# Performance work log

Measured on AMD Instinct MI355X. Metric: run time of the kernel, lower is better.

The kernel has to match this reference:

```python
import jax, jax.numpy as jnp
import numpy as np
from jax import lax
from functools import partial


def _dilate(masks):
    # conv with an all-ones k x k kernel followed by (>0) == binary max-pool dilation
    H = masks.shape[-1]
    k = H // 50
    k = k if k % 2 == 1 else k + 1
    pad = k // 2
    d = lax.reduce_window(masks, -jnp.inf, lax.max, (1, 1, k, k), (1, 1, 1, 1),
                          [(0, 0), (0, 0), (pad, pad), (pad, pad)])
    return (d > 0).astype(masks.dtype)


def _boxes_from_masks(masks):
    # vectorized version of the torch double loop with per-mask torch.where
    N, M, H, W = masks.shape
    b = masks > 0
    any_y = b.any(axis=3)  # (N,M,H)
    any_x = b.any(axis=2)  # (N,M,W)
    ys = jnp.arange(H)
    xs = jnp.arange(W)
    ymin = jnp.min(jnp.where(any_y, ys, H), axis=-1)
    ymax = jnp.max(jnp.where(any_y, ys, -1), axis=-1)
    xmin = jnp.min(jnp.where(any_x, xs, W), axis=-1)
    xmax = jnp.max(jnp.where(any_x, xs, -1), axis=-1)
    x1 = jnp.maximum(0, xmin - 1)
    y1 = jnp.maximum(0, ymin - 1)
    x2 = jnp.minimum(W - 1, xmax + 1)
    y2 = jnp.minimum(H - 1, ymax + 1)
    box = jnp.stack([x1, y1, x2, y2], axis=-1).astype(jnp.float32)  # (N,M,4)
    nonempty = any_y.any(axis=-1)
    return jnp.where(nonempty[..., None], box, 0.0)


def _bilinear(feat, y, x):
    # torchvision roi_align bilinear sampling semantics (aligned=False)
    C, H, W = feat.shape
    valid = (y > -1.0) & (y < H) & (x > -1.0) & (x < W)
    y = jnp.clip(y, 0.0, H - 1.0)
    x = jnp.clip(x, 0.0, W - 1.0)
    y0 = jnp.floor(y).astype(jnp.int32)
    x0 = jnp.floor(x).astype(jnp.int32)
    y1 = jnp.minimum(y0 + 1, H - 1)
    x1 = jnp.minimum(x0 + 1, W - 1)
    ly = y - y0
    lx = x - x0
    hy = 1.0 - ly
    hx = 1.0 - lx
    v00 = feat[:, y0, x0]
    v01 = feat[:, y0, x1]
    v10 = feat[:, y1, x0]
    v11 = feat[:, y1, x1]
    val = hy * hx * v00 + hy * lx * v01 + ly * hx * v10 + ly * lx * v11
    return jnp.where(valid, val, 0.0)


def _roi_align_one(feat, box, R):
    # sampling_ratio=1: one sample at each bin center
    x1, y1, x2, y2 = box
    bw = jnp.maximum(x2 - x1, 1.0) / R
    bh = jnp.maximum(y2 - y1, 1.0) / R
    px = x1 + (jnp.arange(R) + 0.5) * bw
    py = y1 + (jnp.arange(R) + 0.5) * bh
    yg, xg = jnp.meshgrid(py, px, indexing='ij')  # (R,R)
    return _roi_bilinear_wrap(feat, yg, xg)


def _roi_bilinear_wrap(feat, yg, xg):
    return _bilinear(feat, yg, xg)


def _crop_mask_one(mask, box, R):
    # dynamic crop + nearest resize expressed as a single gather
    Hf, Wf = mask.shape
    x1 = jnp.maximum(jnp.floor(box[0]).astype(jnp.int32), 0)
    y1 = jnp.maximum(jnp.floor(box[1]).astype(jnp.int32), 0)
    x2 = jnp.minimum(jnp.floor(box[2]).astype(jnp.int32), Wf - 1)
    y2 = jnp.minimum(jnp.floor(box[3]).astype(jnp.int32), Hf - 1)
    h = y2 - y1 + 1
    w = x2 - x1 + 1
    yi = y1 + (jnp.arange(R) * h) // R  # floor(i*h/R) nearest indices
    xi = x1 + (jnp.arange(R) * w) // R
    crop = mask[yi[:, None], xi[None, :]]
    return jnp.where(crop.sum() > 0, crop, jnp.ones_like(crop))


def _forward(batch_features, batch_masks, R):
    N, C, Hf, Wf = batch_features.shape
    M = batch_masks.shape[1]
    Hi, Wi = batch_masks.shape[-2:]
    masks = _dilate(batch_masks)
    boxes = _boxes_from_masks(masks) * (Hf / Hi)  # feature-map coordinates
    # F.interpolate(mode='nearest') to (Hf,Wf)
    hidx = (jnp.arange(Hf) * Hi) // Hf
    widx = (jnp.arange(Wf) * Wi) // Wf
    masks_small = masks[:, :, hidx, :][:, :, :, widx]  # (N,M,Hf,Wf)
    ra = partial(_roi_align_one, R=R)
    roi_feats = jax.vmap(jax.vmap(ra, (None, 0)), (0, 0))(batch_features, boxes)  # (N,M,C,R,R)
    cm = partial(_crop_mask_one, R=R)
    roi_masks = jax.vmap(jax.vmap(cm, (0, 0)), (0, 0))(masks_small, boxes)  # (N,M,R,R)
    emb = (roi_feats * roi_masks[:, :, None]).reshape(N, M, -1)
    return boxes / Hf, roi_masks, emb


def setup_inputs() -> dict:
    key = jax.random.key(0)
    k1, k2 = jax.random.split(key)
    batch_features = jax.random.normal(k1, (4, 768, 48, 48), dtype=jnp.float32)
    # sparse seed points; dilation (15x15) grows them into blob masks
    batch_masks = (jax.random.uniform(k2, (4, 64, 768, 768)) > 0.99995).astype(jnp.float32)
    return {"batch_features": batch_features, "batch_masks": batch_masks,
            "token_resolution": 8}


def reference(batch_features, batch_masks, token_resolution):
    return _forward(batch_features, batch_masks, int(token_resolution))
```

## Files before the change

### kernel.cpp

```cpp
#include <hip/hip_runtime.h>
#include <hip/hip_bf16.h>

#define N_ 4
#define M_ 64
#define C_ 768
#define HF 48
#define WF 48
#define HWF (HF*WF)
#define HI 768
#define WI 768
#define R_ 8
#define NM (N_*M_)

#define WS_BBOX_OFF   0
#define WS_BF_OFF     4096
#define WS_MS_OFF     8192
#define WS_FEATT_OFF  (1u<<20)
#define MS_PER_MAP    (HF*WF)

#define VEC4_PER_MAP  (HI*WI/4)
#define SCAN_LPT      16
#define SCAN_BX       (VEC4_PER_MAP/(256*SCAN_LPT))

typedef float f32x4 __attribute__((ext_vector_type(4)));

__global__ void init_ws_kernel(int* __restrict__ bbox, unsigned int* __restrict__ ms32) {
    int idx = blockIdx.x * 256 + threadIdx.x;
    int total32 = NM * MS_PER_MAP / 4;
    if (idx < total32) ms32[idx] = 0u;
    if (idx < NM) {
        bbox[idx*4 + 0] = 1 << 30;
        bbox[idx*4 + 1] = -1;
        bbox[idx*4 + 2] = 1 << 30;
        bbox[idx*4 + 3] = -1;
    }
}

__global__ void transpose_feat_kernel(const float* __restrict__ feat,
                                      float* __restrict__ featT) {
    __shared__ float lds[64][65];
    const int n   = blockIdx.z;
    const int hw0 = blockIdx.y * 64;
    const int c0  = blockIdx.x * 64;
    const int t   = threadIdx.x;
    const int lane = t & 63;
    const int grp  = t >> 6;

    #pragma unroll
    for (int i = 0; i < 16; ++i) {
        const int c_l = i * 4 + grp;
        lds[c_l][lane] = feat[((size_t)(n * C_ + c0 + c_l)) * HWF + hw0 + lane];
    }
    __syncthreads();
    #pragma unroll
    for (int i = 0; i < 16; ++i) {
        const int hw_l = i * 4 + grp;
        featT[((size_t)(n * HWF + hw0 + hw_l)) * C_ + c0 + lane] = lds[lane][hw_l];
    }
}

__global__ void scan_masks_kernel(const f32x4* __restrict__ masks,
                                  int* __restrict__ bbox,
                                  unsigned char* __restrict__ msmall) {
    const int nm = blockIdx.y;
    const size_t map_off = (size_t)nm * VEC4_PER_MAP;
    const int chunk = blockIdx.x * (256 * SCAN_LPT);
    int* bb = bbox + nm * 4;
    unsigned char* ms = msmall + nm * MS_PER_MAP;

    #pragma unroll
    for (int k = 0; k < SCAN_LPT; ++k) {
        const int t = chunk + k * 256 + threadIdx.x;
        const f32x4 v = __builtin_nontemporal_load(masks + map_off + t);
        if (v.x > 0.f || v.y > 0.f || v.z > 0.f || v.w > 0.f) {
            const int y  = t / (WI/4);
            const int x4 = (t - y * (WI/4)) * 4;
            const float vv[4] = {v.x, v.y, v.z, v.w};
            #pragma unroll
            for (int q = 0; q < 4; ++q) {
                if (vv[q] > 0.f) {
                    const int x = x4 + q;
                    atomicMin(&bb[0], y);
                    atomicMax(&bb[1], y);
                    atomicMin(&bb[2], x);
                    atomicMax(&bb[3], x);
                    const int i = (y + 7) >> 4;
                    const int j = (x + 7) >> 4;
                    if (((y & 15) != 8) && i < HF && ((x & 15) != 8) && j < WF)
                        ms[i*WF + j] = 1;
                }
            }
        }
    }
}

__global__ void boxes_masks_kernel(const int* __restrict__ bbox,
                                   const unsigned char* __restrict__ msmall,
                                   float* __restrict__ boxes_feat,
                                   float* __restrict__ out) {
    const int nm = blockIdx.x;
    const int tid = threadIdx.x;
    const int ymin = bbox[nm*4+0], ymax = bbox[nm*4+1];
    const int xmin = bbox[nm*4+2], xmax = bbox[nm*4+3];

    float bf0, bf1, bf2, bf3;
    if (ymax < 0) {
        bf0 = bf1 = bf2 = bf3 = 0.f;
    } else {
        bf0 = (float)max(xmin - 8, 0) * 0.0625f;
        bf1 = (float)max(ymin - 8, 0) * 0.0625f;
        bf2 = (float)min(xmax + 8, WI - 1) * 0.0625f;
        bf3 = (float)min(ymax + 8, HI - 1) * 0.0625f;
    }
    if (tid == 0) {
        boxes_feat[nm*4+0] = bf0; boxes_feat[nm*4+1] = bf1;
        boxes_feat[nm*4+2] = bf2; boxes_feat[nm*4+3] = bf3;
        out[nm*4+0] = bf0 * (1.f/HF);
        out[nm*4+1] = bf1 * (1.f/HF);
        out[nm*4+2] = bf2 * (1.f/HF);
        out[nm*4+3] = bf3 * (1.f/HF);
    }

    const int x1i = max((int)floorf(bf0), 0);
    const int y1i = max((int)floorf(bf1), 0);
    const int x2i = min((int)floorf(bf2), WF - 1);
    const int y2i = min((int)floorf(bf3), HF - 1);
    const int h = y2i - y1i + 1;
    const int w = x2i - x1i + 1;
    const int r = tid >> 3, s = tid & 7;
    const int yi = y1i + (r * h) / R_;
    const int xi = x1i + (s * w) / R_;
    const float cv = (float)msmall[nm*MS_PER_MAP + yi*WF + xi];
    const bool nonzero = __any(cv > 0.f);
    out[NM*4 + nm*64 + tid] = nonzero ? cv : 1.f;
}

__global__ void roi_feat_kernel(const float* __restrict__ featT,
                                const float* __restrict__ boxes_feat,
                                const float* __restrict__ roi_masks,
                                float* __restrict__ emb) {
    const int nm = blockIdx.y;
    const int n  = nm >> 6;
    const int c0 = blockIdx.x * 64;
    const int tid = threadIdx.x;

    __shared__ float s_w[4][64];
    __shared__ int   s_a[4][64];
    __shared__ float s_m[64];
    __shared__ float tile[64][65];

    if (tid < 64) {
        const float x1  = boxes_feat[nm*4+0];
        const float y1f = boxes_feat[nm*4+1];
        const float x2  = boxes_feat[nm*4+2];
        const float y2f = boxes_feat[nm*4+3];
        const float bw = fmaxf(x2 - x1, 1.f) * (1.f / R_);
        const float bh = fmaxf(y2f - y1f, 1.f) * (1.f / R_);
        const int r = tid >> 3, s = tid & 7;
        float py = y1f + ((float)r + 0.5f) * bh;
        float px = x1  + ((float)s + 0.5f) * bw;
        py = fminf(fmaxf(py, 0.f), (float)(HF - 1));
        px = fminf(fmaxf(px, 0.f), (float)(WF - 1));
        const int y0 = (int)floorf(py);
        const int x0 = (int)floorf(px);
        const int y1i = min(y0 + 1, HF - 1);
        const int x1i = min(x0 + 1, WF - 1);
        const float ly = py - (float)y0, lx = px - (float)x0;
        const float hy = 1.f - ly,       hx = 1.f - lx;
        s_w[0][tid] = hy * hx;  s_w[1][tid] = hy * lx;
        s_w[2][tid] = ly * hx;  s_w[3][tid] = ly * lx;
        s_a[0][tid] = y0 * WF + x0;   s_a[1][tid] = y0 * WF + x1i;
        s_a[2][tid] = y1i * WF + x0;  s_a[3][tid] = y1i * WF + x1i;
        s_m[tid] = roi_masks[nm * 64 + tid];
    }
    __syncthreads();

    const int c_l = tid & 63;
    const int pg  = tid >> 6;
    const float* fb = featT + (size_t)n * HWF * C_ + c0 + c_l;
    #pragma unroll
    for (int p = 0; p < 16; ++p) {
        const int pos = pg * 16 + p;
        const float v = s_w[0][pos] * fb[(size_t)s_a[0][pos] * C_]
                      + s_w[1][pos] * fb[(size_t)s_a[1][pos] * C_]
                      + s_w[2][pos] * fb[(size_t)s_a[2][pos] * C_]
                      + s_w[3][pos] * fb[(size_t)s_a[3][pos] * C_];
        tile[pos][c_l] = v;
    }
    __syncthreads();

    const int pos = tid & 63;
    #pragma unroll
    for (int i = 0; i < 16; ++i) {
        const int cc = i * 4 + (tid >> 6);
        emb[((size_t)nm * C_ + c0 + cc) * 64 + pos] = tile[pos][cc] * s_m[pos];
    }
}

extern "C" void kernel_launch(void* const* d_in, const int* in_sizes, int n_in,
                              void* d_out, int out_size, void* d_ws, size_t ws_size,
                              hipStream_t stream) {
    const float* feat  = (const float*)d_in[0];
    const float* masks = (const float*)d_in[1];
    float* out = (float*)d_out;

    char* ws = (char*)d_ws;
    int* bbox             = (int*)(ws + WS_BBOX_OFF);
    float* boxes_feat     = (float*)(ws + WS_BF_OFF);
    unsigned char* msmall = (unsigned char*)(ws + WS_MS_OFF);
    float* featT          = (float*)(ws + WS_FEATT_OFF);

    init_ws_kernel<<<(NM*MS_PER_MAP/4 + 255)/256, 256, 0, stream>>>(bbox, (unsigned int*)msmall);

    dim3 gt(C_/64, HWF/64, N_);
    transpose_feat_kernel<<<gt, 256, 0, stream>>>(feat, featT);

    dim3 g1(SCAN_BX, NM);
    scan_masks_kernel<<<g1, 256, 0, stream>>>((const f32x4*)masks, bbox, msmall);

    boxes_masks_kernel<<<NM, 64, 0, stream>>>(bbox, msmall, boxes_feat, out);

    const float* roi_masks = out + NM*4;
    float* emb = out + NM*4 + NM*R_*R_;
    dim3 g2(C_/64, NM);
    roi_feat_kernel<<<g2, 256, 0, stream>>>(featT, boxes_feat, roi_masks, emb);
}
```

Measured before the change: 157.2 us.

## Fuse mask scan with feature transpose and fold box/mask logic into ROI kernel

Merges the mask scan and the feature transpose into a single launch that dispatches on block index, so both run in one grid. The box computation and mask cropping move into the ROI kernel, and the separate boxes/masks kernel goes away. The init kernel is replaced by a memset, made possible by re-encoding the min/max bbox atomics as atomicMax on offset unsigned values so that zero is a valid initial state. The aim is to cut kernel launch count and inter-kernel gaps; the cost is that every ROI block now recomputes the box and mask values.

```diff
diff --git a/kernel.cpp b/kernel.cpp
--- a/kernel.cpp
+++ b/kernel.cpp
@@ -13,132 +13,90 @@
 #define NM (N_*M_)
 
 #define WS_BBOX_OFF   0
-#define WS_BF_OFF     4096
-#define WS_MS_OFF     8192
+#define WS_MS_OFF     4096
 #define WS_FEATT_OFF  (1u<<20)
 #define MS_PER_MAP    (HF*WF)
+#define WS_ZERO_BYTES (WS_MS_OFF + NM*MS_PER_MAP)
 
 #define VEC4_PER_MAP  (HI*WI/4)
 #define SCAN_LPT      16
 #define SCAN_BX       (VEC4_PER_MAP/(256*SCAN_LPT))
+#define SCAN_BLOCKS   (NM*SCAN_BX)
+#define TRANS_BLOCKS  ((C_/64)*(HWF/64)*N_)
 
 typedef float f32x4 __attribute__((ext_vector_type(4)));
 
-__global__ void init_ws_kernel(int* __restrict__ bbox, unsigned int* __restrict__ ms32) {
-    int idx = blockIdx.x * 256 + threadIdx.x;
-    int total32 = NM * MS_PER_MAP / 4;
-    if (idx < total32) ms32[idx] = 0u;
-    if (idx < NM) {
-        bbox[idx*4 + 0] = 1 << 30;
-        bbox[idx*4 + 1] = -1;
-        bbox[idx*4 + 2] = 1 << 30;
-        bbox[idx*4 + 3] = -1;
-    }
-}
-
-__global__ void transpose_feat_kernel(const float* __restrict__ feat,
-                                      float* __restrict__ featT) {
+__global__ void scan_trans_kernel(const f32x4* __restrict__ masks,
+                                  const float* __restrict__ feat,
+                                  unsigned int* __restrict__ bbox,
+                                  unsigned char* __restrict__ msmall,
+                                  float* __restrict__ featT) {
     __shared__ float lds[64][65];
-    const int n   = blockIdx.z;
-    const int hw0 = blockIdx.y * 64;
-    const int c0  = blockIdx.x * 64;
-    const int t   = threadIdx.x;
-    const int lane = t & 63;
-    const int grp  = t >> 6;
-
-    #pragma unroll
-    for (int i = 0; i < 16; ++i) {
-        const int c_l = i * 4 + grp;
-        lds[c_l][lane] = feat[((size_t)(n * C_ + c0 + c_l)) * HWF + hw0 + lane];
-    }
-    __syncthreads();
-    #pragma unroll
-    for (int i = 0; i < 16; ++i) {
-        const int hw_l = i * 4 + grp;
-        featT[((size_t)(n * HWF + hw0 + hw_l)) * C_ + c0 + lane] = lds[lane][hw_l];
-    }
-}
-
-__global__ void scan_masks_kernel(const f32x4* __restrict__ masks,
-                                  int* __restrict__ bbox,
-                                  unsigned char* __restrict__ msmall) {
-    const int nm = blockIdx.y;
-    const size_t map_off = (size_t)nm * VEC4_PER_MAP;
-    const int chunk = blockIdx.x * (256 * SCAN_LPT);
-    int* bb = bbox + nm * 4;
-    unsigned char* ms = msmall + nm * MS_PER_MAP;
-
-    #pragma unroll
-    for (int k = 0; k < SCAN_LPT; ++k) {
-        const int t = chunk + k * 256 + threadIdx.x;
-        const f32x4 v = __builtin_nontemporal_load(masks + map_off + t);
-        if (v.x > 0.f || v.y > 0.f || v.z > 0.f || v.w > 0.f) {
-            const int y  = t / (WI/4);
-            const int x4 = (t - y * (WI/4)) * 4;
-            const float vv[4] = {v.x, v.y, v.z, v.w};
-            #pragma unroll
-            for (int q = 0; q < 4; ++q) {
-                if (vv[q] > 0.f) {
-                    const int x = x4 + q;
-                    atomicMin(&bb[0], y);
-                    atomicMax(&bb[1], y);
-                    atomicMin(&bb[2], x);
-                    atomicMax(&bb[3], x);
-                    const int i = (y + 7) >> 4;
-                    const int j = (x + 7) >> 4;
-                    if (((y & 15) != 8) && i < HF && ((x & 15) != 8) && j < WF)
-                        ms[i*WF + j] = 1;
+    const int bid = blockIdx.x;
+    const int tid = threadIdx.x;
+
+    if (bid < SCAN_BLOCKS) {
+        const int nm = bid / SCAN_BX;
+        const int bx = bid - nm * SCAN_BX;
+        const size_t map_off = (size_t)nm * VEC4_PER_MAP;
+        const int chunk = bx * (256 * SCAN_LPT);
+        unsigned int* bb = bbox + nm * 4;
+        unsigned char* ms = msmall + nm * MS_PER_MAP;
+
+        #pragma unroll
+        for (int k = 0; k < SCAN_LPT; ++k) {
+            const int t = chunk + k * 256 + tid;
+            const f32x4 v = __builtin_nontemporal_load(masks + map_off + t);
+            if (v.x > 0.f || v.y > 0.f || v.z > 0.f || v.w > 0.f) {
+                const int y  = t / (WI/4);
+                const int x4 = (t - y * (WI/4)) * 4;
+                const float vv[4] = {v.x, v.y, v.z, v.w};
+                #pragma unroll
+                for (int q = 0; q < 4; ++q) {
+                    if (vv[q] > 0.f) {
+                        const int x = x4 + q;
+                        atomicMax(&bb[0], (unsigned int)(HI - y));
+                        atomicMax(&bb[1], (unsigned int)(y + 1));
+                        atomicMax(&bb[2], (unsigned int)(WI - x));
+                        atomicMax(&bb[3], (unsigned int)(x + 1));
+                        const int i = (y + 7) >> 4;
+                        const int j = (x + 7) >> 4;
+                        if (((y & 15) != 8) && i < HF && ((x & 15) != 8) && j < WF)
+                            ms[i*WF + j] = 1;
+                    }
                 }
             }
         }
+    } else {
+        const int tb  = bid - SCAN_BLOCKS;
+        const int ct  = tb % (C_/64);
+        const int tmp = tb / (C_/64);
+        const int hwt = tmp % (HWF/64);
+        const int n   = tmp / (HWF/64);
+        const int hw0 = hwt * 64;
+        const int c0  = ct * 64;
+        const int lane = tid & 63;
+        const int grp  = tid >> 6;
+
+        #pragma unroll
+        for (int i = 0; i < 16; ++i) {
+            const int c_l = i * 4 + grp;
+            lds[c_l][lane] = __builtin_nontemporal_load(
+                feat + ((size_t)(n * C_ + c0 + c_l)) * HWF + hw0 + lane);
+        }
+        __syncthreads();
+        #pragma unroll
+        for (int i = 0; i < 16; ++i) {
+            const int hw_l = i * 4 + grp;
+            featT[((size_t)(n * HWF + hw0 + hw_l)) * C_ + c0 + lane] = lds[lane][hw_l];
+        }
     }
 }
 
-__global__ void boxes_masks_kernel(const int* __restrict__ bbox,
-                                   const unsigned char* __restrict__ msmall,
-                                   float* __restrict__ boxes_feat,
-                                   float* __restrict__ out) {
-    const int nm = blockIdx.x;
-    const int tid = threadIdx.x;
-    const int ymin = bbox[nm*4+0], ymax = bbox[nm*4+1];
-    const int xmin = bbox[nm*4+2], xmax = bbox[nm*4+3];
-
-    float bf0, bf1, bf2, bf3;
-    if (ymax < 0) {
-        bf0 = bf1 = bf2 = bf3 = 0.f;
-    } else {
-        bf0 = (float)max(xmin - 8, 0) * 0.0625f;
-        bf1 = (float)max(ymin - 8, 0) * 0.0625f;
-        bf2 = (float)min(xmax + 8, WI - 1) * 0.0625f;
-        bf3 = (float)min(ymax + 8, HI - 1) * 0.0625f;
-    }
-    if (tid == 0) {
-        boxes_feat[nm*4+0] = bf0; boxes_feat[nm*4+1] = bf1;
-        boxes_feat[nm*4+2] = bf2; boxes_feat[nm*4+3] = bf3;
-        out[nm*4+0] = bf0 * (1.f/HF);
-        out[nm*4+1] = bf1 * (1.f/HF);
-        out[nm*4+2] = bf2 * (1.f/HF);
-        out[nm*4+3] = bf3 * (1.f/HF);
-    }
-
-    const int x1i = max((int)floorf(bf0), 0);
-    const int y1i = max((int)floorf(bf1), 0);
-    const int x2i = min((int)floorf(bf2), WF - 1);
-    const int y2i = min((int)floorf(bf3), HF - 1);
-    const int h = y2i - y1i + 1;
-    const int w = x2i - x1i + 1;
-    const int r = tid >> 3, s = tid & 7;
-    const int yi = y1i + (r * h) / R_;
-    const int xi = x1i + (s * w) / R_;
-    const float cv = (float)msmall[nm*MS_PER_MAP + yi*WF + xi];
-    const bool nonzero = __any(cv > 0.f);
-    out[NM*4 + nm*64 + tid] = nonzero ? cv : 1.f;
-}
-
-__global__ void roi_feat_kernel(const float* __restrict__ featT,
-                                const float* __restrict__ boxes_feat,
-                                const float* __restrict__ roi_masks,
-                                float* __restrict__ emb) {
+__global__ void roi_fused_kernel(const float* __restrict__ featT,
+                                 const unsigned int* __restrict__ bbox,
+                                 const unsigned char* __restrict__ msmall,
+                                 float* __restrict__ out) {
     const int nm = blockIdx.y;
     const int n  = nm >> 6;
     const int c0 = blockIdx.x * 64;
@@ -150,15 +108,44 @@
     __shared__ float tile[64][65];
 
     if (tid < 64) {
-        const float x1  = boxes_feat[nm*4+0];
-        const float y1f = boxes_feat[nm*4+1];
-        const float x2  = boxes_feat[nm*4+2];
-        const float y2f = boxes_feat[nm*4+3];
-        const float bw = fmaxf(x2 - x1, 1.f) * (1.f / R_);
-        const float bh = fmaxf(y2f - y1f, 1.f) * (1.f / R_);
+        const uint4 bb = ((const uint4*)bbox)[nm];
+        float bf0, bf1, bf2, bf3;
+        if (bb.y == 0u) {
+            bf0 = bf1 = bf2 = bf3 = 0.f;
+        } else {
+            const int ymin = HI - (int)bb.x, ymax = (int)bb.y - 1;
+            const int xmin = WI - (int)bb.z, xmax = (int)bb.w - 1;
+            bf0 = (float)max(xmin - 8, 0) * 0.0625f;
+            bf1 = (float)max(ymin - 8, 0) * 0.0625f;
+            bf2 = (float)min(xmax + 8, WI - 1) * 0.0625f;
+            bf3 = (float)min(ymax + 8, HI - 1) * 0.0625f;
+        }
+        if (blockIdx.x == 0 && tid == 0) {
+            out[nm*4+0] = bf0 * (1.f/HF);
+            out[nm*4+1] = bf1 * (1.f/HF);
+            out[nm*4+2] = bf2 * (1.f/HF);
+            out[nm*4+3] = bf3 * (1.f/HF);
+        }
+
+        const int x1c = max((int)floorf(bf0), 0);
+        const int y1c = max((int)floorf(bf1), 0);
+        const int x2c = min((int)floorf(bf2), WF - 1);
+        const int y2c = min((int)floorf(bf3), HF - 1);
+        const int h = y2c - y1c + 1;
+        const int w = x2c - x1c + 1;
         const int r = tid >> 3, s = tid & 7;
-        float py = y1f + ((float)r + 0.5f) * bh;
-        float px = x1  + ((float)s + 0.5f) * bw;
+        const int yi = y1c + (r * h) / R_;
+        const int xi = x1c + (s * w) / R_;
+        const float cv = (float)msmall[nm*MS_PER_MAP + yi*WF + xi];
+        const float m = __any(cv > 0.f) ? cv : 1.f;
+        s_m[tid] = m;
+        if (blockIdx.x == 0)
+            out[NM*4 + nm*64 + tid] = m;
+
+        const float bw = fmaxf(bf2 - bf0, 1.f) * (1.f / R_);
+        const float bh = fmaxf(bf3 - bf1, 1.f) * (1.f / R_);
+        float py = bf1 + ((float)r + 0.5f) * bh;
+        float px = bf0 + ((float)s + 0.5f) * bw;
         py = fminf(fmaxf(py, 0.f), (float)(HF - 1));
         px = fminf(fmaxf(px, 0.f), (float)(WF - 1));
         const int y0 = (int)floorf(py);
@@ -171,7 +158,6 @@
         s_w[2][tid] = ly * hx;  s_w[3][tid] = ly * lx;
         s_a[0][tid] = y0 * WF + x0;   s_a[1][tid] = y0 * WF + x1i;
         s_a[2][tid] = y1i * WF + x0;  s_a[3][tid] = y1i * WF + x1i;
-        s_m[tid] = roi_masks[nm * 64 + tid];
     }
     __syncthreads();
 
@@ -189,6 +175,7 @@
     }
     __syncthreads();
 
+    float* emb = out + NM*4 + NM*R_*R_;
     const int pos = tid & 63;
     #pragma unroll
     for (int i = 0; i < 16; ++i) {
@@ -205,23 +192,15 @@
     float* out = (float*)d_out;
 
     char* ws = (char*)d_ws;
-    int* bbox             = (int*)(ws + WS_BBOX_OFF);
-    float* boxes_feat     = (float*)(ws + WS_BF_OFF);
+    unsigned int* bbox    = (unsigned int*)(ws + WS_BBOX_OFF);
     unsigned char* msmall = (unsigned char*)(ws + WS_MS_OFF);
     float* featT          = (float*)(ws + WS_FEATT_OFF);
 
-    init_ws_kernel<<<(NM*MS_PER_MAP/4 + 255)/256, 256, 0, stream>>>(bbox, (unsigned int*)msmall);
-
-    dim3 gt(C_/64, HWF/64, N_);
-    transpose_feat_kernel<<<gt, 256, 0, stream>>>(feat, featT);
-
-    dim3 g1(SCAN_BX, NM);
-    scan_masks_kernel<<<g1, 256, 0, stream>>>((const f32x4*)masks, bbox, msmall);
-
-    boxes_masks_kernel<<<NM, 64, 0, stream>>>(bbox, msmall, boxes_feat, out);
-
-    const float* roi_masks = out + NM*4;
-    float* emb = out + NM*4 + NM*R_*R_;
+    hipMemsetAsync(ws, 0, WS_ZERO_BYTES, stream);
+
+    scan_trans_kernel<<<SCAN_BLOCKS + TRANS_BLOCKS, 256, 0, stream>>>(
+        (const f32x4*)masks, feat, bbox, msmall, featT);
+
     dim3 g2(C_/64, NM);
-    roi_feat_kernel<<<g2, 256, 0, stream>>>(featT, boxes_feat, roi_masks, emb);
+    roi_fused_kernel<<<g2, 256, 0, stream>>>(featT, bbox, msmall, out);
 }
```

Result: no change. 157.9 us (+0.4%).
